# Performance work log

Measured on AMD Instinct MI355X. Metric: run time of the kernel, lower is better.

The kernel has to match this reference:

```python
import jax, jax.numpy as jnp
import numpy as np

B, L, H = 2, 1024, 768
DI, N, K, R = 1536, 16, 4, 48


def setup_inputs() -> dict:
    key = jax.random.key(0)
    ks = jax.random.split(key, 10)
    s = 0.02
    inp = {
        "x": jax.random.normal(ks[0], (B, L, H), jnp.float32),
        "in_up_w": jax.random.normal(ks[1], (2 * DI * 4, H), jnp.float32) * s,
        "in_down_w": jax.random.normal(ks[2], (2 * DI, 2 * DI * 4), jnp.float32) * s,
        "conv_w": jax.random.normal(ks[3], (DI, 1, K), jnp.float32) * 0.5,
        "conv_b": jnp.zeros((DI,), jnp.float32),
        "x_proj_w": jax.random.normal(ks[4], (R + 2 * N, DI), jnp.float32) * s,
        "dt_w": jax.random.normal(ks[5], (DI, R), jnp.float32) * s,
        "dt_b": jnp.full((DI,), -4.0, jnp.float32) + jax.random.normal(ks[6], (DI,), jnp.float32) * 0.1,
        "A_log": jnp.log(jnp.broadcast_to(jnp.arange(1, N + 1, dtype=jnp.float32)[None, :], (DI, N))),
        "D": jnp.ones((DI,), jnp.float32),
        "out_up_w": jax.random.normal(ks[7], (4 * DI, DI), jnp.float32) * s,
        "out_down_w": jax.random.normal(ks[8], (H, 4 * DI), jnp.float32) * s,
    }
    return inp


def reference(x, in_up_w, in_down_w, conv_w, conv_b, x_proj_w, dt_w, dt_b,
              A_log, D, out_up_w, out_down_w):
    act = jax.nn.silu
    # in_up_proj -> act -> in_down_proj  (use_bias=False)
    proj = act(x @ in_up_w.T) @ in_down_w.T          # [B, L, 2*DI]
    proj = proj.transpose(0, 2, 1)                   # [B, 2*DI, L]
    hs, gate = jnp.split(proj, 2, axis=1)            # each [B, DI, L]

    # depthwise causal conv1d (pad left K-1, truncate to L) + SiLU
    k = conv_w.shape[-1]
    c = hs.shape[1]
    y = jax.lax.conv_general_dilated(
        hs, conv_w, window_strides=(1,), padding=[(k - 1, 0)],
        feature_group_count=c, dimension_numbers=("NCH", "OIH", "NCH"))
    hs = act(y + conv_b[None, :, None])              # [B, DI, L]

    # x_proj -> split into dt / B / C
    ssm_p = jnp.einsum("bdl,kd->blk", hs, x_proj_w)  # [B, L, R+2N]
    r = dt_w.shape[1]
    n = A_log.shape[1]
    ts, Bm, Cm = jnp.split(ssm_p, [r, r + n], axis=-1)
    dt = jax.nn.softplus(ts @ dt_w.T + dt_b)         # [B, L, DI]
    dt = dt.transpose(0, 2, 1)                       # [B, DI, L]

    A = -jnp.exp(A_log)                              # [DI, N]
    dA = jnp.exp(dt[..., None] * A[None, :, None, :])        # [B, DI, L, N]
    dBu = dt[..., None] * Bm[:, None, :, :] * hs[..., None]  # [B, DI, L, N]

    def step(s, inps):
        dA_t, dBu_t, C_t = inps          # [B,DI,N], [B,DI,N], [B,N]
        s = dA_t * s + dBu_t
        return s, jnp.einsum("bdn,bn->bd", s, C_t)

    s0 = jnp.zeros((x.shape[0], c, n), x.dtype)
    _, ys = jax.lax.scan(
        step, s0,
        (dA.transpose(2, 0, 1, 3), dBu.transpose(2, 0, 1, 3), Cm.transpose(1, 0, 2)))
    yscan = ys.transpose(1, 2, 0)                    # [B, DI, L]

    yscan = yscan + hs * D[None, :, None]
    yscan = yscan * act(gate)

    # out_up_proj -> act -> out_down_proj (use_bias=False)
    out = act(yscan.transpose(0, 2, 1) @ out_up_w.T) @ out_down_w.T  # [B, L, H]
    return out
```

## Files before the change

kernel.cpp:

```cpp
#include <hip/hip_runtime.h>
#include <hip/hip_bf16.h>
#include <cstdint>

#define B_   2
#define L_   1024
#define H_   768
#define DI_  1536
#define DI2_ 3072
#define DUP_ 12288
#define DOUT_ 6144
#define N_   16
#define R_   48
#define SPW  128
#define BL_  2048
#define C_   64
#define CL_  16

typedef __bf16 bf16x8 __attribute__((ext_vector_type(8)));
typedef float  f32x4  __attribute__((ext_vector_type(4)));
typedef unsigned int u32;

__device__ __forceinline__ float silu_f(float v) {
    return v / (1.f + __expf(-v));
}

__device__ __forceinline__ void async_ld16(const void* g, void* lds) {
    __builtin_amdgcn_global_load_lds(
        (const __attribute__((address_space(1))) u32*)g,
        (__attribute__((address_space(3))) u32*)lds, 16, 0, 0);
}

__device__ __forceinline__ void cvt8(const float* __restrict__ s, __bf16* __restrict__ d, int i)
{
    const float4 a = *(const float4*)(s + i);
    const float4 b = *(const float4*)(s + i + 4);
    bf16x8 v;
    v[0] = (__bf16)a.x; v[1] = (__bf16)a.y; v[2] = (__bf16)a.z; v[3] = (__bf16)a.w;
    v[4] = (__bf16)b.x; v[5] = (__bf16)b.y; v[6] = (__bf16)b.z; v[7] = (__bf16)b.w;
    *(bf16x8*)(d + i) = v;
}

__global__ void prep1(const float* __restrict__ x, const float* __restrict__ wup,
                      const float* __restrict__ wdn,
                      __bf16* __restrict__ xb, __bf16* __restrict__ wupb,
                      __bf16* __restrict__ wdnb)
{
    const int bid = blockIdx.x;
    if (bid < 768)            cvt8(x,   xb,   (bid * 256 + threadIdx.x) * 8);
    else if (bid < 5376)      cvt8(wup, wupb, ((bid - 768) * 256 + threadIdx.x) * 8);
    else                      cvt8(wdn, wdnb, ((bid - 5376) * 256 + threadIdx.x) * 8);
}

__global__ void prep2(const float* __restrict__ woup, const float* __restrict__ wodn,
                      const float* __restrict__ xp, const float* __restrict__ dtw,
                      __bf16* __restrict__ woupb, __bf16* __restrict__ wodnb,
                      __bf16* __restrict__ xppad, float* __restrict__ dtwT)
{
    const int bid = blockIdx.x;
    if (bid < 4608)        cvt8(woup, woupb, (bid * 256 + threadIdx.x) * 8);
    else if (bid < 6912)   cvt8(wodn, wodnb, ((bid - 4608) * 256 + threadIdx.x) * 8);
    else if (bid < 7008) {
        const int i = ((bid - 6912) * 256 + threadIdx.x) * 8;
        const int j = i / DI_;
        bf16x8 v;
        if (j < 80) {
            const float4 a = *(const float4*)(xp + i);
            const float4 b = *(const float4*)(xp + i + 4);
            v[0] = (__bf16)a.x; v[1] = (__bf16)a.y; v[2] = (__bf16)a.z; v[3] = (__bf16)a.w;
            v[4] = (__bf16)b.x; v[5] = (__bf16)b.y; v[6] = (__bf16)b.z; v[7] = (__bf16)b.w;
        } else {
            for (int k = 0; k < 8; ++k) v[k] = (__bf16)0.f;
        }
        *(bf16x8*)(xppad + i) = v;
    } else {
        const int i = (bid - 7008) * 256 + threadIdx.x;
        const int r = i / DI_, d = i % DI_;
        dtwT[i] = dtw[(size_t)d * R_ + r];
    }
}

template<int EPI, int ATOMIC, int SWZ, typename OutT>
__global__ __launch_bounds__(256) void gemm_bf16(
    const __bf16* __restrict__ A, const __bf16* __restrict__ W, OutT* __restrict__ O,
    int M, int N, int Kslice, int lda, int ldw, int ldo)
{
    constexpr int BM = 128, BN = 128, BK = 32;
    __shared__ __bf16 As[BM * BK];
    __shared__ __bf16 Bs[BN * BK];

    const int tid  = threadIdx.x;
    int bx = blockIdx.x, by = blockIdx.y;
    if (SWZ) {
        const int nxy  = gridDim.x * gridDim.y;
        const int flat = blockIdx.x + gridDim.x * blockIdx.y;
        const int qq   = nxy >> 3;
        const int s    = (flat & 7) * qq + (flat >> 3);
        bx = s % gridDim.x; by = s / gridDim.x;
    }
    const int bm   = bx * BM;
    const int bn   = by * BN;
    const int kbase = blockIdx.z * Kslice;
    if (ATOMIC == 0) O += (size_t)blockIdx.z * (size_t)M * ldo;

    const int wave = tid >> 6, lane = tid & 63;
    const int wm = (wave >> 1) * 64, wn = (wave & 1) * 64;
    const int quad = lane >> 4, tr = lane & 15;

    const int srow = tid >> 2;
    const int skc  = ((tid & 3) ^ ((srow >> 1) & 3)) * 8;
    const __bf16* Ag0 = A + (size_t)(bm + srow) * lda + kbase + skc;
    const __bf16* Ag1 = A + (size_t)(bm + srow + 64) * lda + kbase + skc;
    const __bf16* Wg0 = W + (size_t)(bn + srow) * ldw + kbase + skc;
    const __bf16* Wg1 = W + (size_t)(bn + srow + 64) * ldw + kbase + skc;
    __bf16* Al0 = &As[tid * 8];
    __bf16* Al1 = &As[2048 + tid * 8];
    __bf16* Bl0 = &Bs[tid * 8];
    __bf16* Bl1 = &Bs[2048 + tid * 8];

    const int fsw = (quad ^ ((tr >> 1) & 3)) * 8;
    const __bf16* arp = &As[(wm + tr) * BK + fsw];
    const __bf16* brp = &Bs[(wn + tr) * BK + fsw];

    f32x4 acc[4][4];
#pragma unroll
    for (int i = 0; i < 4; ++i)
#pragma unroll
        for (int j = 0; j < 4; ++j) acc[i][j] = (f32x4){0.f, 0.f, 0.f, 0.f};

    for (int k0 = 0; k0 < Kslice; k0 += BK) {
        __syncthreads();
        async_ld16(Ag0 + k0, Al0);
        async_ld16(Ag1 + k0, Al1);
        async_ld16(Wg0 + k0, Bl0);
        async_ld16(Wg1 + k0, Bl1);
        __syncthreads();

        bf16x8 af[4], bfv[4];
#pragma unroll
        for (int i = 0; i < 4; ++i) af[i]  = *(const bf16x8*)(arp + i * 16 * BK);
#pragma unroll
        for (int j = 0; j < 4; ++j) bfv[j] = *(const bf16x8*)(brp + j * 16 * BK);
#pragma unroll
        for (int i = 0; i < 4; ++i)
#pragma unroll
            for (int j = 0; j < 4; ++j)
                acc[i][j] = __builtin_amdgcn_mfma_f32_16x16x32_bf16(af[i], bfv[j], acc[i][j], 0, 0, 0);
    }

#pragma unroll
    for (int i = 0; i < 4; ++i) {
        const int row = bm + wm + i * 16 + quad * 4;
#pragma unroll
        for (int j = 0; j < 4; ++j) {
            const int col = bn + wn + j * 16 + tr;
            OutT* op = O + (size_t)row * ldo + col;
#pragma unroll
            for (int r = 0; r < 4; ++r) {
                float v = acc[i][j][r];
                if (EPI == 1) v = silu_f(v);
                if (ATOMIC == 1) atomicAdd((float*)(op + (size_t)r * ldo), v);
                else             op[(size_t)r * ldo] = (OutT)v;
            }
        }
    }
}

__global__ void reduce_sp(const float* __restrict__ SPp, float* __restrict__ SPb)
{
    const int i = (blockIdx.x * 256 + threadIdx.x) * 4;
    float4 a = *(const float4*)(SPp + i);
#pragma unroll
    for (int z = 1; z < 8; ++z) {
        const float4 b = *(const float4*)(SPp + (size_t)z * (BL_ * SPW) + i);
        a.x += b.x; a.y += b.y; a.z += b.z; a.w += b.w;
    }
    *(float4*)(SPb + i) = a;
}

__global__ void reduce_out(const float* __restrict__ OP, float* __restrict__ out)
{
    const int i = (blockIdx.x * 256 + threadIdx.x) * 4;
    float4 a = *(const float4*)(OP + i);
#pragma unroll
    for (int z = 1; z < 4; ++z) {
        const float4 b = *(const float4*)(OP + (size_t)z * (BL_ * H_) + i);
        a.x += b.x; a.y += b.y; a.z += b.z; a.w += b.w;
    }
    *(float4*)(out + i) = a;
}

__global__ void conv_kernel(const float* __restrict__ P0, const float* __restrict__ P1,
                            const float* __restrict__ cw, const float* __restrict__ cb,
                            __bf16* __restrict__ HSb)
{
    const int t = blockIdx.x * blockDim.x + threadIdx.x;
    const int d = t % DI_;
    const int bl = t / DI_;
    const int l = bl % L_;
    const float4 w = *(const float4*)(cw + (size_t)d * 4);
    const float wk[4] = {w.x, w.y, w.z, w.w};
    float acc = cb[d];
#pragma unroll
    for (int k = 0; k < 4; ++k) {
        const int ls = l - 3 + k;
        if (ls >= 0) {
            const size_t idx = (size_t)(bl - l + ls) * DI2_ + d;
            acc += wk[k] * (P0[idx] + P1[idx]);
        }
    }
    HSb[t] = (__bf16)silu_f(acc);
}

__global__ void dt_kernel(const float* __restrict__ SP, const float* __restrict__ dtwT,
                          const float* __restrict__ dtb, float* __restrict__ DT)
{
    const int t = blockIdx.x * blockDim.x + threadIdx.x;
    const int d = t % DI_;
    const int bl = t / DI_;
    const float* ts = SP + (size_t)bl * SPW;
    float s = dtb[d];
#pragma unroll
    for (int r4 = 0; r4 < R_ / 4; ++r4) {
        const float4 tv = *(const float4*)(ts + r4 * 4);
        const float* wp = dtwT + (size_t)r4 * 4 * DI_ + d;
        s += tv.x * wp[0] + tv.y * wp[DI_] + tv.z * wp[2 * DI_] + tv.w * wp[3 * DI_];
    }
    DT[t] = (s > 20.f) ? s : log1pf(__expf(s));
}

__global__ __launch_bounds__(256) void scan_pass1(
    const float* __restrict__ DT, const __bf16* __restrict__ HSb,
    const float* __restrict__ SP, const float* __restrict__ A_log,
    float* __restrict__ Aprod, float* __restrict__ Bacc)
{
    const int t = blockIdx.x * blockDim.x + threadIdx.x;
    const int d = t % DI_;
    const int y = t / DI_;
    const int c = y % C_;
    const int b = y / C_;
    float A[N_], s[N_], ap[N_];
    {
        const float4* alp = (const float4*)(A_log + (size_t)d * N_);
        const float4 a0 = alp[0], a1 = alp[1], a2 = alp[2], a3 = alp[3];
        const float av[N_] = {a0.x,a0.y,a0.z,a0.w, a1.x,a1.y,a1.z,a1.w,
                              a2.x,a2.y,a2.z,a2.w, a3.x,a3.y,a3.z,a3.w};
#pragma unroll
        for (int n = 0; n < N_; ++n) { A[n] = -__expf(av[n]); s[n] = 0.f; ap[n] = 1.f; }
    }
    for (int il = 0; il < CL_; ++il) {
        const size_t bl = (size_t)b * L_ + c * CL_ + il;
        const float dt = DT[bl * DI_ + d];
        const float hs = (float)HSb[bl * DI_ + d];
        const float4* Bp = (const float4*)(SP + bl * SPW + R_);
        const float4 b0 = Bp[0], b1 = Bp[1], b2 = Bp[2], b3 = Bp[3];
        const float Bv[N_] = {b0.x,b0.y,b0.z,b0.w, b1.x,b1.y,b1.z,b1.w,
                              b2.x,b2.y,b2.z,b2.w, b3.x,b3.y,b3.z,b3.w};
        const float dh = dt * hs;
#pragma unroll
        for (int n = 0; n < N_; ++n) {
            const float dA = __expf(dt * A[n]);
            s[n] = fmaf(dA, s[n], dh * Bv[n]);
            ap[n] *= dA;
        }
    }
    float4* Ap = (float4*)(Aprod + (size_t)t * N_);
    float4* Bc = (float4*)(Bacc  + (size_t)t * N_);
    Ap[0] = make_float4(ap[0], ap[1], ap[2], ap[3]);
    Ap[1] = make_float4(ap[4], ap[5], ap[6], ap[7]);
    Ap[2] = make_float4(ap[8], ap[9], ap[10], ap[11]);
    Ap[3] = make_float4(ap[12], ap[13], ap[14], ap[15]);
    Bc[0] = make_float4(s[0], s[1], s[2], s[3]);
    Bc[1] = make_float4(s[4], s[5], s[6], s[7]);
    Bc[2] = make_float4(s[8], s[9], s[10], s[11]);
    Bc[3] = make_float4(s[12], s[13], s[14], s[15]);
}

__global__ __launch_bounds__(256) void scan_pass2(
    const float* __restrict__ Aprod, const float* __restrict__ Bacc,
    float* __restrict__ Sinit)
{
    const int t = blockIdx.x * blockDim.x + threadIdx.x;
    const int n = t & (N_ - 1);
    const int d = (t >> 4) % DI_;
    const int b = (t >> 4) / DI_;
    float s = 0.f;
    for (int c = 0; c < C_; ++c) {
        const size_t idx = (((size_t)b * C_ + c) * DI_ + d) * N_ + n;
        Sinit[idx] = s;
        s = fmaf(Aprod[idx], s, Bacc[idx]);
    }
}

__global__ __launch_bounds__(256) void scan_pass3(
    const float* __restrict__ DT, const __bf16* __restrict__ HSb,
    const float* __restrict__ SP, const float* __restrict__ P0,
    const float* __restrict__ P1, const float* __restrict__ A_log,
    const float* __restrict__ Dv, const float* __restrict__ Sinit,
    __bf16* __restrict__ Y)
{
    const int t = blockIdx.x * blockDim.x + threadIdx.x;
    const int d = t % DI_;
    const int y = t / DI_;
    const int c = y % C_;
    const int b = y / C_;
    float A[N_], s[N_];
    {
        const float4* alp = (const float4*)(A_log + (size_t)d * N_);
        const float4 a0 = alp[0], a1 = alp[1], a2 = alp[2], a3 = alp[3];
        const float av[N_] = {a0.x,a0.y,a0.z,a0.w, a1.x,a1.y,a1.z,a1.w,
                              a2.x,a2.y,a2.z,a2.w, a3.x,a3.y,a3.z,a3.w};
#pragma unroll
        for (int n = 0; n < N_; ++n) A[n] = -__expf(av[n]);
    }
    {
        const float4* sp = (const float4*)(Sinit + (size_t)t * N_);
        const float4 s0 = sp[0], s1 = sp[1], s2 = sp[2], s3 = sp[3];
        s[0]=s0.x; s[1]=s0.y; s[2]=s0.z; s[3]=s0.w;
        s[4]=s1.x; s[5]=s1.y; s[6]=s1.z; s[7]=s1.w;
        s[8]=s2.x; s[9]=s2.y; s[10]=s2.z; s[11]=s2.w;
        s[12]=s3.x; s[13]=s3.y; s[14]=s3.z; s[15]=s3.w;
    }
    const float Dd = Dv[d];
    for (int il = 0; il < CL_; ++il) {
        const size_t bl = (size_t)b * L_ + c * CL_ + il;
        const float dt = DT[bl * DI_ + d];
        const float hs = (float)HSb[bl * DI_ + d];
        const float4* Bp = (const float4*)(SP + bl * SPW + R_);
        const float4 b0 = Bp[0], b1 = Bp[1], b2 = Bp[2], b3 = Bp[3];
        const float4 c0 = Bp[4], c1 = Bp[5], c2 = Bp[6], c3 = Bp[7];
        const float Bv[N_] = {b0.x,b0.y,b0.z,b0.w, b1.x,b1.y,b1.z,b1.w,
                              b2.x,b2.y,b2.z,b2.w, b3.x,b3.y,b3.z,b3.w};
        const float Cv[N_] = {c0.x,c0.y,c0.z,c0.w, c1.x,c1.y,c1.z,c1.w,
                              c2.x,c2.y,c2.z,c2.w, c3.x,c3.y,c3.z,c3.w};
        const float dh = dt * hs;
        float acc = 0.f;
#pragma unroll
        for (int n = 0; n < N_; ++n) {
            const float dA = __expf(dt * A[n]);
            s[n] = fmaf(dA, s[n], dh * Bv[n]);
            acc = fmaf(s[n], Cv[n], acc);
        }
        const size_t gidx = bl * DI2_ + DI_ + d;
        const float g = P0[gidx] + P1[gidx];
        Y[bl * DI_ + d] = (__bf16)((acc + hs * Dd) * silu_f(g));
    }
}

extern "C" void kernel_launch(void* const* d_in, const int* in_sizes, int n_in,
                              void* d_out, int out_size, void* d_ws, size_t ws_size,
                              hipStream_t stream) {
    const float* x        = (const float*)d_in[0];
    const float* w_up     = (const float*)d_in[1];
    const float* w_down   = (const float*)d_in[2];
    const float* conv_w   = (const float*)d_in[3];
    const float* conv_b   = (const float*)d_in[4];
    const float* x_proj_w = (const float*)d_in[5];
    const float* dt_w     = (const float*)d_in[6];
    const float* dt_b     = (const float*)d_in[7];
    const float* A_log    = (const float*)d_in[8];
    const float* Dvec     = (const float*)d_in[9];
    const float* w_oup    = (const float*)d_in[10];
    const float* w_odown  = (const float*)d_in[11];
    float* out = (float*)d_out;

    char* base = (char*)d_ws;
    __bf16* x_b      = (__bf16*)base;
    __bf16* wup_b    = (__bf16*)(base + 3145728);
    float*  P0       = (float*)base;
    float*  P1       = (float*)(base + 25165824);
    char* r2 = base + 50331648;
    __bf16* wdown_b  = (__bf16*)r2;
    __bf16* HSb      = (__bf16*)r2;
    float*  SPb      = (float*)(r2 + 6291456);
    float*  SPp      = (float*)(r2 + 7340032);
    float*  DTb      = (float*)(r2 + 15728640);
    __bf16* Yb       = (__bf16*)(r2 + 28311552);
    __bf16* XPpad    = (__bf16*)(r2 + 34603008);
    float*  dtwT     = (float*)(r2 + 34996224);
    __bf16* woup_b   = (__bf16*)(r2 + 35291136);
    __bf16* wodown_b = (__bf16*)(r2 + 54165504);
    char* r3 = r2 + 75497472;
    __bf16* U1b      = (__bf16*)r3;
    __bf16* U2b      = (__bf16*)r3;
    float*  Aprod    = (float*)r3;
    float*  Bacc     = (float*)(r3 + 12582912);
    float*  Sinit    = (float*)(r3 + 25165824);
    float*  OP       = (float*)(r3 + 25165824);

    prep1<<<23808, 256, 0, stream>>>(x, w_up, w_down, x_b, wup_b, wdown_b);

    gemm_bf16<1, 0, 0, __bf16><<<dim3(16, 96, 1), 256, 0, stream>>>(
        x_b, wup_b, U1b, BL_, DUP_, H_, H_, H_, DUP_);

    gemm_bf16<0, 0, 1, float><<<dim3(16, 24, 2), 256, 0, stream>>>(
        U1b, wdown_b, P0, BL_, DI2_, DUP_ / 2, DUP_, DUP_, DI2_);

    prep2<<<7296, 256, 0, stream>>>(w_oup, w_odown, x_proj_w, dt_w,
                                    woup_b, wodown_b, XPpad, dtwT);

    conv_kernel<<<(BL_ * DI_) / 256, 256, 0, stream>>>(P0, P1, conv_w, conv_b, HSb);

    gemm_bf16<0, 0, 0, float><<<dim3(16, 1, 8), 256, 0, stream>>>(
        HSb, XPpad, SPp, BL_, SPW, DI_ / 8, DI_, DI_, SPW);
    reduce_sp<<<(BL_ * SPW) / 1024, 256, 0, stream>>>(SPp, SPb);

    dt_kernel<<<(BL_ * DI_) / 256, 256, 0, stream>>>(SPb, dtwT, dt_b, DTb);

    scan_pass1<<<(B_ * C_ * DI_) / 256, 256, 0, stream>>>(DTb, HSb, SPb, A_log, Aprod, Bacc);
    scan_pass2<<<(B_ * DI_ * N_) / 256, 256, 0, stream>>>(Aprod, Bacc, Sinit);
    scan_pass3<<<(B_ * C_ * DI_) / 256, 256, 0, stream>>>(
        DTb, HSb, SPb, P0, P1, A_log, Dvec, Sinit, Yb);

    gemm_bf16<1, 0, 0, __bf16><<<dim3(16, 48, 1), 256, 0, stream>>>(
        Yb, woup_b, U2b, BL_, DOUT_, DI_, DI_, DI_, DOUT_);

    gemm_bf16<0, 0, 0, float><<<dim3(16, 6, 4), 256, 0, stream>>>(
        U2b, wodown_b, OP, BL_, H_, DOUT_ / 4, DOUT_, DOUT_, H_);
    reduce_out<<<(BL_ * H_) / 1024, 256, 0, stream>>>(OP, out);
}
```

Baseline: 820.9 us.

## Fuse weight conversions into GEMM and conv launches, raise out-proj split-K

```diff
diff --git a/kernel.cpp b/kernel.cpp
--- a/kernel.cpp
+++ b/kernel.cpp
@@ -40,27 +40,146 @@
     *(bf16x8*)(d + i) = v;
 }
 
+template<int EPI, int ATOMIC, typename OutT>
+__device__ __forceinline__ void gemm_tile(
+    const __bf16* __restrict__ A, const __bf16* __restrict__ W, OutT* __restrict__ O,
+    int Kslice, int lda, int ldw, int ldo, int bm, int bn, int kbase)
+{
+    constexpr int BK = 32;
+    __shared__ __bf16 As[128 * BK];
+    __shared__ __bf16 Bs[128 * BK];
+
+    const int tid  = threadIdx.x;
+    const int wave = tid >> 6, lane = tid & 63;
+    const int wm = (wave >> 1) * 64, wn = (wave & 1) * 64;
+    const int quad = lane >> 4, tr = lane & 15;
+
+    const int srow = tid >> 2;
+    const int skc  = ((tid & 3) ^ ((srow >> 1) & 3)) * 8;
+    const __bf16* Ag0 = A + (size_t)(bm + srow) * lda + kbase + skc;
+    const __bf16* Ag1 = A + (size_t)(bm + srow + 64) * lda + kbase + skc;
+    const __bf16* Wg0 = W + (size_t)(bn + srow) * ldw + kbase + skc;
+    const __bf16* Wg1 = W + (size_t)(bn + srow + 64) * ldw + kbase + skc;
+    __bf16* Al0 = &As[tid * 8];
+    __bf16* Al1 = &As[2048 + tid * 8];
+    __bf16* Bl0 = &Bs[tid * 8];
+    __bf16* Bl1 = &Bs[2048 + tid * 8];
+
+    const int fsw = (quad ^ ((tr >> 1) & 3)) * 8;
+    const __bf16* arp = &As[(wm + tr) * BK + fsw];
+    const __bf16* brp = &Bs[(wn + tr) * BK + fsw];
+
+    f32x4 acc[4][4];
+#pragma unroll
+    for (int i = 0; i < 4; ++i)
+#pragma unroll
+        for (int j = 0; j < 4; ++j) acc[i][j] = (f32x4){0.f, 0.f, 0.f, 0.f};
+
+    for (int k0 = 0; k0 < Kslice; k0 += BK) {
+        __syncthreads();
+        async_ld16(Ag0 + k0, Al0);
+        async_ld16(Ag1 + k0, Al1);
+        async_ld16(Wg0 + k0, Bl0);
+        async_ld16(Wg1 + k0, Bl1);
+        __syncthreads();
+
+        bf16x8 af[4], bfv[4];
+#pragma unroll
+        for (int i = 0; i < 4; ++i) af[i]  = *(const bf16x8*)(arp + i * 16 * BK);
+#pragma unroll
+        for (int j = 0; j < 4; ++j) bfv[j] = *(const bf16x8*)(brp + j * 16 * BK);
+#pragma unroll
+        for (int i = 0; i < 4; ++i)
+#pragma unroll
+            for (int j = 0; j < 4; ++j)
+                acc[i][j] = __builtin_amdgcn_mfma_f32_16x16x32_bf16(af[i], bfv[j], acc[i][j], 0, 0, 0);
+    }
+
+#pragma unroll
+    for (int i = 0; i < 4; ++i) {
+        const int row = bm + wm + i * 16 + quad * 4;
+#pragma unroll
+        for (int j = 0; j < 4; ++j) {
+            const int col = bn + wn + j * 16 + tr;
+            OutT* op = O + (size_t)row * ldo + col;
+#pragma unroll
+            for (int r = 0; r < 4; ++r) {
+                float v = acc[i][j][r];
+                if (EPI == 1) v = silu_f(v);
+                if (ATOMIC == 1) atomicAdd((float*)(op + (size_t)r * ldo), v);
+                else             op[(size_t)r * ldo] = (OutT)v;
+            }
+        }
+    }
+}
+
+template<int EPI, int ATOMIC, typename OutT>
+__global__ __launch_bounds__(256) void gemm_bf16(
+    const __bf16* __restrict__ A, const __bf16* __restrict__ W, OutT* __restrict__ O,
+    int M, int N, int Kslice, int lda, int ldw, int ldo)
+{
+    if (ATOMIC == 0) O += (size_t)blockIdx.z * (size_t)M * ldo;
+    gemm_tile<EPI, ATOMIC, OutT>(A, W, O, Kslice, lda, ldw, ldo,
+                                 blockIdx.x * 128, blockIdx.y * 128,
+                                 blockIdx.z * Kslice);
+}
+
 __global__ void prep1(const float* __restrict__ x, const float* __restrict__ wup,
-                      const float* __restrict__ wdn,
-                      __bf16* __restrict__ xb, __bf16* __restrict__ wupb,
-                      __bf16* __restrict__ wdnb)
+                      __bf16* __restrict__ xb, __bf16* __restrict__ wupb)
 {
     const int bid = blockIdx.x;
-    if (bid < 768)            cvt8(x,   xb,   (bid * 256 + threadIdx.x) * 8);
-    else if (bid < 5376)      cvt8(wup, wupb, ((bid - 768) * 256 + threadIdx.x) * 8);
-    else                      cvt8(wdn, wdnb, ((bid - 5376) * 256 + threadIdx.x) * 8);
-}
-
-__global__ void prep2(const float* __restrict__ woup, const float* __restrict__ wodn,
-                      const float* __restrict__ xp, const float* __restrict__ dtw,
-                      __bf16* __restrict__ woupb, __bf16* __restrict__ wodnb,
-                      __bf16* __restrict__ xppad, float* __restrict__ dtwT)
+    if (bid < 768) cvt8(x,   xb,   (bid * 256 + threadIdx.x) * 8);
+    else           cvt8(wup, wupb, ((bid - 768) * 256 + threadIdx.x) * 8);
+}
+
+__global__ __launch_bounds__(256) void g1_fused(
+    const __bf16* __restrict__ xb, const __bf16* __restrict__ wupb,
+    __bf16* __restrict__ U1b,
+    const float* __restrict__ wdn, __bf16* __restrict__ wdnb)
 {
     const int bid = blockIdx.x;
-    if (bid < 4608)        cvt8(woup, woupb, (bid * 256 + threadIdx.x) * 8);
-    else if (bid < 6912)   cvt8(wodn, wodnb, ((bid - 4608) * 256 + threadIdx.x) * 8);
-    else if (bid < 7008) {
-        const int i = ((bid - 6912) * 256 + threadIdx.x) * 8;
+    if (bid < 1536) {
+        const int bx = bid & 15, by = bid >> 4;
+        gemm_tile<1, 0, __bf16>(xb, wupb, U1b, H_, H_, H_, DUP_,
+                                bx * 128, by * 128, 0);
+    } else {
+        cvt8(wdn, wdnb, ((bid - 1536) * 256 + threadIdx.x) * 8);
+    }
+}
+
+__global__ void conv_prep2(const float* __restrict__ P0, const float* __restrict__ P1,
+                           const float* __restrict__ cw, const float* __restrict__ cb,
+                           __bf16* __restrict__ HSb,
+                           const float* __restrict__ woup, const float* __restrict__ wodn,
+                           const float* __restrict__ xp, const float* __restrict__ dtw,
+                           __bf16* __restrict__ woupb, __bf16* __restrict__ wodnb,
+                           __bf16* __restrict__ xppad, float* __restrict__ dtwT)
+{
+    const int bid = blockIdx.x;
+    if (bid < 12288) {
+        const int t = bid * 256 + threadIdx.x;
+        const int d = t % DI_;
+        const int bl = t / DI_;
+        const int l = bl % L_;
+        const float4 w = *(const float4*)(cw + (size_t)d * 4);
+        const float wk[4] = {w.x, w.y, w.z, w.w};
+        float acc = cb[d];
+#pragma unroll
+        for (int k = 0; k < 4; ++k) {
+            const int ls = l - 3 + k;
+            if (ls >= 0) {
+                const size_t idx = (size_t)(bl - l + ls) * DI2_ + d;
+                acc += wk[k] * (P0[idx] + P1[idx]);
+            }
+        }
+        HSb[t] = (__bf16)silu_f(acc);
+        return;
+    }
+    const int pid = bid - 12288;
+    if (pid < 4608)        cvt8(woup, woupb, (pid * 256 + threadIdx.x) * 8);
+    else if (pid < 6912)   cvt8(wodn, wodnb, ((pid - 4608) * 256 + threadIdx.x) * 8);
+    else if (pid < 7008) {
+        const int i = ((pid - 6912) * 256 + threadIdx.x) * 8;
         const int j = i / DI_;
         bf16x8 v;
         if (j < 80) {
@@ -73,95 +192,9 @@
         }
         *(bf16x8*)(xppad + i) = v;
     } else {
-        const int i = (bid - 7008) * 256 + threadIdx.x;
+        const int i = (pid - 7008) * 256 + threadIdx.x;
         const int r = i / DI_, d = i % DI_;
         dtwT[i] = dtw[(size_t)d * R_ + r];
-    }
-}
-
-template<int EPI, int ATOMIC, int SWZ, typename OutT>
-__global__ __launch_bounds__(256) void gemm_bf16(
-    const __bf16* __restrict__ A, const __bf16* __restrict__ W, OutT* __restrict__ O,
-    int M, int N, int Kslice, int lda, int ldw, int ldo)
-{
-    constexpr int BM = 128, BN = 128, BK = 32;
-    __shared__ __bf16 As[BM * BK];
-    __shared__ __bf16 Bs[BN * BK];
-
-    const int tid  = threadIdx.x;
-    int bx = blockIdx.x, by = blockIdx.y;
-    if (SWZ) {
-        const int nxy  = gridDim.x * gridDim.y;
-        const int flat = blockIdx.x + gridDim.x * blockIdx.y;
-        const int qq   = nxy >> 3;
-        const int s    = (flat & 7) * qq + (flat >> 3);
-        bx = s % gridDim.x; by = s / gridDim.x;
-    }
-    const int bm   = bx * BM;
-    const int bn   = by * BN;
-    const int kbase = blockIdx.z * Kslice;
-    if (ATOMIC == 0) O += (size_t)blockIdx.z * (size_t)M * ldo;
-
-    const int wave = tid >> 6, lane = tid & 63;
-    const int wm = (wave >> 1) * 64, wn = (wave & 1) * 64;
-    const int quad = lane >> 4, tr = lane & 15;
-
-    const int srow = tid >> 2;
-    const int skc  = ((tid & 3) ^ ((srow >> 1) & 3)) * 8;
-    const __bf16* Ag0 = A + (size_t)(bm + srow) * lda + kbase + skc;
-    const __bf16* Ag1 = A + (size_t)(bm + srow + 64) * lda + kbase + skc;
-    const __bf16* Wg0 = W + (size_t)(bn + srow) * ldw + kbase + skc;
-    const __bf16* Wg1 = W + (size_t)(bn + srow + 64) * ldw + kbase + skc;
-    __bf16* Al0 = &As[tid * 8];
-    __bf16* Al1 = &As[2048 + tid * 8];
-    __bf16* Bl0 = &Bs[tid * 8];
-    __bf16* Bl1 = &Bs[2048 + tid * 8];
-
-    const int fsw = (quad ^ ((tr >> 1) & 3)) * 8;
-    const __bf16* arp = &As[(wm + tr) * BK + fsw];
-    const __bf16* brp = &Bs[(wn + tr) * BK + fsw];
-
-    f32x4 acc[4][4];
-#pragma unroll
-    for (int i = 0; i < 4; ++i)
-#pragma unroll
-        for (int j = 0; j < 4; ++j) acc[i][j] = (f32x4){0.f, 0.f, 0.f, 0.f};
-
-    for (int k0 = 0; k0 < Kslice; k0 += BK) {
-        __syncthreads();
-        async_ld16(Ag0 + k0, Al0);
-        async_ld16(Ag1 + k0, Al1);
-        async_ld16(Wg0 + k0, Bl0);
-        async_ld16(Wg1 + k0, Bl1);
-        __syncthreads();
-
-        bf16x8 af[4], bfv[4];
-#pragma unroll
-        for (int i = 0; i < 4; ++i) af[i]  = *(const bf16x8*)(arp + i * 16 * BK);
-#pragma unroll
-        for (int j = 0; j < 4; ++j) bfv[j] = *(const bf16x8*)(brp + j * 16 * BK);
-#pragma unroll
-        for (int i = 0; i < 4; ++i)
-#pragma unroll
-            for (int j = 0; j < 4; ++j)
-                acc[i][j] = __builtin_amdgcn_mfma_f32_16x16x32_bf16(af[i], bfv[j], acc[i][j], 0, 0, 0);
-    }
-
-#pragma unroll
-    for (int i = 0; i < 4; ++i) {
-        const int row = bm + wm + i * 16 + quad * 4;
-#pragma unroll
-        for (int j = 0; j < 4; ++j) {
-            const int col = bn + wn + j * 16 + tr;
-            OutT* op = O + (size_t)row * ldo + col;
-#pragma unroll
-            for (int r = 0; r < 4; ++r) {
-                float v = acc[i][j][r];
-                if (EPI == 1) v = silu_f(v);
-                if (ATOMIC == 1) atomicAdd((float*)(op + (size_t)r * ldo), v);
-                else             op[(size_t)r * ldo] = (OutT)v;
-            }
-        }
     }
 }
 
@@ -182,33 +215,11 @@
     const int i = (blockIdx.x * 256 + threadIdx.x) * 4;
     float4 a = *(const float4*)(OP + i);
 #pragma unroll
-    for (int z = 1; z < 4; ++z) {
+    for (int z = 1; z < 8; ++z) {
         const float4 b = *(const float4*)(OP + (size_t)z * (BL_ * H_) + i);
         a.x += b.x; a.y += b.y; a.z += b.z; a.w += b.w;
     }
     *(float4*)(out + i) = a;
-}
-
-__global__ void conv_kernel(const float* __restrict__ P0, const float* __restrict__ P1,
-                            const float* __restrict__ cw, const float* __restrict__ cb,
-                            __bf16* __restrict__ HSb)
-{
-    const int t = blockIdx.x * blockDim.x + threadIdx.x;
-    const int d = t % DI_;
-    const int bl = t / DI_;
-    const int l = bl % L_;
-    const float4 w = *(const float4*)(cw + (size_t)d * 4);
-    const float wk[4] = {w.x, w.y, w.z, w.w};
-    float acc = cb[d];
-#pragma unroll
-    for (int k = 0; k < 4; ++k) {
-        const int ls = l - 3 + k;
-        if (ls >= 0) {
-            const size_t idx = (size_t)(bl - l + ls) * DI2_ + d;
-            acc += wk[k] * (P0[idx] + P1[idx]);
-        }
-    }
-    HSb[t] = (__bf16)silu_f(acc);
 }
 
 __global__ void dt_kernel(const float* __restrict__ SP, const float* __restrict__ dtwT,
@@ -368,6 +379,7 @@
     __bf16* wup_b    = (__bf16*)(base + 3145728);
     float*  P0       = (float*)base;
     float*  P1       = (float*)(base + 25165824);
+    float*  OP       = (float*)base;
     char* r2 = base + 50331648;
     __bf16* wdown_b  = (__bf16*)r2;
     __bf16* HSb      = (__bf16*)r2;
@@ -385,22 +397,19 @@
     float*  Aprod    = (float*)r3;
     float*  Bacc     = (float*)(r3 + 12582912);
     float*  Sinit    = (float*)(r3 + 25165824);
-    float*  OP       = (float*)(r3 + 25165824);
-
-    prep1<<<23808, 256, 0, stream>>>(x, w_up, w_down, x_b, wup_b, wdown_b);
-
-    gemm_bf16<1, 0, 0, __bf16><<<dim3(16, 96, 1), 256, 0, stream>>>(
-        x_b, wup_b, U1b, BL_, DUP_, H_, H_, H_, DUP_);
-
-    gemm_bf16<0, 0, 1, float><<<dim3(16, 24, 2), 256, 0, stream>>>(
+
+    prep1<<<5376, 256, 0, stream>>>(x, w_up, x_b, wup_b);
+
+    g1_fused<<<19968, 256, 0, stream>>>(x_b, wup_b, U1b, w_down, wdown_b);
+
+    gemm_bf16<0, 0, float><<<dim3(16, 24, 2), 256, 0, stream>>>(
         U1b, wdown_b, P0, BL_, DI2_, DUP_ / 2, DUP_, DUP_, DI2_);
 
-    prep2<<<7296, 256, 0, stream>>>(w_oup, w_odown, x_proj_w, dt_w,
-                                    woup_b, wodown_b, XPpad, dtwT);
-
-    conv_kernel<<<(BL_ * DI_) / 256, 256, 0, stream>>>(P0, P1, conv_w, conv_b, HSb);
-
-    gemm_bf16<0, 0, 0, float><<<dim3(16, 1, 8), 256, 0, stream>>>(
+    conv_prep2<<<19584, 256, 0, stream>>>(P0, P1, conv_w, conv_b, HSb,
+                                          w_oup, w_odown, x_proj_w, dt_w,
+                                          woup_b, wodown_b, XPpad, dtwT);
+
+    gemm_bf16<0, 0, float><<<dim3(16, 1, 8), 256, 0, stream>>>(
         HSb, XPpad, SPp, BL_, SPW, DI_ / 8, DI_, DI_, SPW);
     reduce_sp<<<(BL_ * SPW) / 1024, 256, 0, stream>>>(SPp, SPb);
 
@@ -411,10 +420,10 @@
     scan_pass3<<<(B_ * C_ * DI_) / 256, 256, 0, stream>>>(
         DTb, HSb, SPb, P0, P1, A_log, Dvec, Sinit, Yb);
 
-    gemm_bf16<1, 0, 0, __bf16><<<dim3(16, 48, 1), 256, 0, stream>>>(
+    gemm_bf16<1, 0, __bf16><<<dim3(16, 48, 1), 256, 0, stream>>>(
         Yb, woup_b, U2b, BL_, DOUT_, DI_, DI_, DI_, DOUT_);
 
-    gemm_bf16<0, 0, 0, float><<<dim3(16, 6, 4), 256, 0, stream>>>(
-        U2b, wodown_b, OP, BL_, H_, DOUT_ / 4, DOUT_, DOUT_, H_);
+    gemm_bf16<0, 0, float><<<dim3(16, 6, 8), 256, 0, stream>>>(
+        U2b, wodown_b, OP, BL_, H_, DOUT_ / 8, DOUT_, DOUT_, H_);
     reduce_out<<<(BL_ * H_) / 1024, 256, 0, stream>>>(OP, out);
 }
```

Measured after the change: 786.2 us. -4.2%, faster.
